# Performance work log

Measured on AMD Instinct MI355X. Metric: run time of the kernel, lower is better.

Reference implementation:

```python
import jax, jax.numpy as jnp
import numpy as np

NX, NY = 8192, 8192
FX, FY = 1024, 1024
EMB, EMB_OUT = 512, 512


def setup_inputs() -> dict:
    key = jax.random.key(0)
    ks = jax.random.split(key, 8)
    s = lambda f: 1.0 / np.sqrt(f)
    return {
        "x": jax.random.normal(ks[0], (NX, FX), jnp.float32),
        "y": jax.random.normal(ks[1], (NY, FY), jnp.float32),
        "Wx": jax.random.uniform(ks[2], (FX, EMB), jnp.float32, -s(FX), s(FX)),
        "bx": jax.random.uniform(ks[3], (EMB,), jnp.float32, -s(FX), s(FX)),
        "Wy": jax.random.uniform(ks[4], (FY, EMB), jnp.float32, -s(FY), s(FY)),
        "by": jax.random.uniform(ks[5], (EMB,), jnp.float32, -s(FY), s(FY)),
        "Wg": jax.random.uniform(ks[6], (EMB, EMB_OUT), jnp.float32, -s(EMB), s(EMB)),
        "bg": jax.random.uniform(ks[7], (EMB_OUT,), jnp.float32, -s(EMB), s(EMB)),
    }


def reference(x, y, Wx, bx, Wy, by, Wg, bg):
    # Linear projections: [Nx, emb], [Ny, emb]
    xp = x @ Wx + bx
    yp = y @ Wy + by
    # Pairwise affinity (Dice-coefficient style normalization)
    A_ = xp @ yp.T                              # [Nx, Ny]
    Dcol = jnp.sum(xp * xp, axis=1)[:, None]    # ||x_i||^2, diag of xp@xp.T
    Drow = jnp.sum(yp * yp, axis=1)[None, :]    # ||y_j||^2, diag of yp@yp.T
    A = 2.0 * A_ / (Dcol + Drow)                # [Nx, Ny]
    # Weighted aggregation over x nodes, then ReLU MLP
    gwf = A.T @ xp                              # [Ny, emb]
    return jax.nn.relu(gwf @ Wg + bg)           # [Ny, emb_out]
```

## Files before the change

kernel.cpp:

```cpp
#include <hip/hip_runtime.h>
#include <hip/hip_bf16.h>


typedef __attribute__((ext_vector_type(8))) short bf16x8;
typedef __attribute__((ext_vector_type(4))) short bf16x4;
typedef __attribute__((ext_vector_type(4))) float f32x4;

__device__ __forceinline__ short f2b(float f) {
    unsigned int u = __builtin_bit_cast(unsigned int, f);
    unsigned int r = (u + 0x7fffu + ((u >> 16) & 1u)) >> 16;
    return (short)r;
}
__device__ __forceinline__ float b2f(short s) {
    unsigned int u = ((unsigned int)(unsigned short)s) << 16;
    return __builtin_bit_cast(float, u);
}

__device__ __forceinline__ void cp16(const void* g, void* l) {
    __builtin_amdgcn_global_load_lds(
        (const __attribute__((address_space(1))) void*)g,
        (__attribute__((address_space(3))) void*)l, 16, 0, 0);
}

constexpr int EPI_XP = 0;
constexpr int EPI_BF = 1;
constexpr int EPI_AT = 2;

template<int EPI, int TM, int TN, int WVN>
__device__ __forceinline__ void gemm_core(
    const short* __restrict__ A, int lda,
    const short* __restrict__ Bt, int ldb,
    int N, int K, int bm, int bn, int kbase,
    const float* __restrict__ bias,
    short* __restrict__ outb,
    float* __restrict__ Dacc,
    const float* __restrict__ Drow, const float* __restrict__ Dcol)
{
    constexpr int WN  = WVN;
    constexpr int WM  = 4 / WN;
    constexpr int FRN = TN / WN / 16;
    constexpr int FRM = TM / WM / 16;
    __shared__ __align__(16) short As[TM * 32];
    __shared__ __align__(16) short Bs[TN * 32];

    const int tid  = threadIdx.x;
    const int wave = tid >> 6;
    const int lane = tid & 63;
    const int quad = lane >> 4;
    const int l15  = lane & 15;
    const int wn   = (wave % WN) * (FRN * 16);
    const int wm   = (wave / WN) * (FRM * 16);

    f32x4 acc[FRM][FRN];
#pragma unroll
    for (int i = 0; i < FRM; i++)
#pragma unroll
        for (int j = 0; j < FRN; j++) acc[i][j] = f32x4{0.f, 0.f, 0.f, 0.f};

    for (int k0 = kbase; k0 < kbase + K; k0 += 32) {
#pragma unroll
        for (int s = 0; s < TM / 64; s++) {
            const int seg = tid + 256 * s;
            const int row = seg >> 2, c8 = seg & 3;
            const int gg  = c8 ^ (row & 3);
            cp16(&A[(size_t)(bm + row) * lda + k0 + gg * 8], &As[seg * 8]);
        }
#pragma unroll
        for (int s = 0; s < TN / 64; s++) {
            const int seg = tid + 256 * s;
            const int row = seg >> 2, c8 = seg & 3;
            const int gg  = c8 ^ (row & 3);
            cp16(&Bt[(size_t)(bn + row) * ldb + k0 + gg * 8], &Bs[seg * 8]);
        }
        __syncthreads();

        bf16x8 a[FRM], b[FRN];
#pragma unroll
        for (int i = 0; i < FRM; i++) {
            const int row = wm + i * 16 + l15;
            a[i] = *(const bf16x8*)&As[row * 32 + ((quad ^ (row & 3)) << 3)];
        }
#pragma unroll
        for (int j = 0; j < FRN; j++) {
            const int row = wn + j * 16 + l15;
            b[j] = *(const bf16x8*)&Bs[row * 32 + ((quad ^ (row & 3)) << 3)];
        }
#pragma unroll
        for (int i = 0; i < FRM; i++)
#pragma unroll
            for (int j = 0; j < FRN; j++)
                acc[i][j] = __builtin_amdgcn_mfma_f32_16x16x32_bf16(a[i], b[j], acc[i][j], 0, 0, 0);
        __syncthreads();
    }

#pragma unroll
    for (int im = 0; im < FRM; ++im) {
#pragma unroll
        for (int r = 0; r < 4; ++r) {
            const int gm = bm + wm + im * 16 + quad * 4 + r;
            if (EPI == EPI_XP) {
                float s = 0.f;
#pragma unroll
                for (int jn = 0; jn < FRN; ++jn) {
                    const int gn = bn + wn + jn * 16 + l15;
                    const float v = acc[im][jn][r] + bias[gn];
                    outb[(size_t)gm * N + gn] = f2b(v);
                    s += v * v;
                }
#pragma unroll
                for (int m = 1; m < 16; m <<= 1) s += __shfl_xor(s, m, 64);
                if (l15 == 0) atomicAdd(&Dacc[gm], s);
            } else if (EPI == EPI_BF) {
#pragma unroll
                for (int jn = 0; jn < FRN; ++jn) {
                    const int gn = bn + wn + jn * 16 + l15;
                    outb[(size_t)gm * N + gn] = f2b(acc[im][jn][r]);
                }
            } else {
                const float dy = Drow[gm];
#pragma unroll
                for (int jn = 0; jn < FRN; ++jn) {
                    const int gn = bn + wn + jn * 16 + l15;
                    const float v = 2.f * acc[im][jn][r] * __builtin_amdgcn_rcpf(Dcol[gn] + dy);
                    outb[(size_t)gm * N + gn] = f2b(v);
                }
            }
        }
    }
}

__global__ __launch_bounds__(256)
void k_proj(const short* __restrict__ A, const short* __restrict__ Bt,
            const float* __restrict__ bias, short* __restrict__ outb,
            float* __restrict__ Dacc)
{
    gemm_core<EPI_XP, 64, 128, 2>(A, 1024, Bt, 1024, 512, 1024,
                                  blockIdx.y * 64, blockIdx.x * 128, 0,
                                  bias, outb, Dacc, nullptr, nullptr);
}

__global__ __launch_bounds__(256)
void k_zT(const short* __restrict__ WgT, const short* __restrict__ xpb,
          short* __restrict__ zT)
{
    gemm_core<EPI_BF, 64, 128, 2>(WgT, 512, xpb, 512, 8192, 512,
                                  blockIdx.y * 64, blockIdx.x * 128, 0,
                                  nullptr, zT, nullptr, nullptr, nullptr);
}

__global__ __launch_bounds__(256, 2)
void k_aff(const short* __restrict__ ypb, const short* __restrict__ xpb,
           short* __restrict__ At, const float* __restrict__ Dy,
           const float* __restrict__ Dx)
{
    const int flat = blockIdx.x;
    const int xcd = flat & 7;
    const int q   = flat >> 3;
    const int st  = q >> 5;
    const int w   = q & 31;
    const int s   = xcd * 8 + st;
    const int bx  = (s & 7) * 4 + (w & 3);
    const int by  = (s >> 3) * 8 + (w >> 2);
    gemm_core<EPI_AT, 128, 256, 2>(ypb, 512, xpb, 512, 8192, 512,
                                   by * 128, bx * 256, 0,
                                   nullptr, At, nullptr, Dy, Dx);
}

__global__ __launch_bounds__(256)
void k_agg(const short* __restrict__ At, const short* __restrict__ zT,
           short* __restrict__ p0, short* __restrict__ p1)
{
    const int flat = blockIdx.x;
    const int xcd = flat & 7;
    const int q   = flat >> 3;
    const int g   = xcd * 16 + (q >> 2);
    const int bm  = (g >> 1) * 128;
    const int z   = g & 1;
    const int bn  = (q & 3) * 128;
    short* outb = z ? p1 : p0;
    gemm_core<EPI_BF, 128, 128, 2>(At, 8192, zT, 8192, 512, 4096,
                                   bm, bn, z * 4096,
                                   nullptr, outb, nullptr, nullptr, nullptr);
}

__global__ __launch_bounds__(256)
void k_fin(const short* __restrict__ p0, const short* __restrict__ p1,
           const float* __restrict__ bg, float* __restrict__ out)
{
    const int idx = (blockIdx.x * 256 + threadIdx.x) * 8;
    const int col = idx & 511;
    const bf16x8 a = *(const bf16x8*)&p0[idx];
    const bf16x8 b = *(const bf16x8*)&p1[idx];
    const f32x4 g0 = *(const f32x4*)&bg[col];
    const f32x4 g1 = *(const f32x4*)&bg[col + 4];
    f32x4 o0, o1;
#pragma unroll
    for (int e = 0; e < 4; ++e) {
        o0[e] = fmaxf(b2f(a[e]) + b2f(b[e]) + g0[e], 0.f);
        o1[e] = fmaxf(b2f(a[e + 4]) + b2f(b[e + 4]) + g1[e], 0.f);
    }
    *(f32x4*)&out[idx]     = o0;
    *(f32x4*)&out[idx + 4] = o1;
}

__global__ __launch_bounds__(256)
void k_cvt(const float* __restrict__ in, short* __restrict__ out)
{
    const int i = (blockIdx.x * 256 + threadIdx.x) * 4;
    const float4 v = *(const float4*)&in[i];
    bf16x4 b;
    b[0] = f2b(v.x); b[1] = f2b(v.y); b[2] = f2b(v.z); b[3] = f2b(v.w);
    *(bf16x4*)&out[i] = b;
}

__global__ __launch_bounds__(256)
void transpose_f32_bf16(const float* __restrict__ in, short* __restrict__ out, int R, int C)
{
    __shared__ short t[32][33];
    const int tx = threadIdx.x, ty = threadIdx.y;
    const int bx = blockIdx.x * 32, by = blockIdx.y * 32;
#pragma unroll
    for (int i = 0; i < 32; i += 8)
        t[ty + i][tx] = f2b(in[(size_t)(by + ty + i) * C + bx + tx]);
    __syncthreads();
#pragma unroll
    for (int i = 0; i < 32; i += 8)
        out[(size_t)(bx + ty + i) * R + by + tx] = t[tx][ty + i];
}

extern "C" void kernel_launch(void* const* d_in, const int* in_sizes, int n_in,
                              void* d_out, int out_size, void* d_ws, size_t ws_size,
                              hipStream_t stream)
{
    const float* x  = (const float*)d_in[0];
    const float* y  = (const float*)d_in[1];
    const float* Wx = (const float*)d_in[2];
    const float* bx = (const float*)d_in[3];
    const float* Wy = (const float*)d_in[4];
    const float* by = (const float*)d_in[5];
    const float* Wg = (const float*)d_in[6];
    const float* bg = (const float*)d_in[7];
    float* out = (float*)d_out;

    char* p = (char*)d_ws;
    short* At   = (short*)p;
    short* xb   = (short*)p;
    short* yb   = (short*)(p + (size_t)8192 * 1024 * 2);
    p += (size_t)8192 * 8192 * 2;
    short* xpb  = (short*)p; p += (size_t)8192 * 512 * 2;
    short* ypb  = (short*)p; p += (size_t)8192 * 512 * 2;
    short* zT   = (short*)p; p += (size_t)512 * 8192 * 2;
    short* WxT  = (short*)p; p += (size_t)512 * 1024 * 2;
    short* WyT  = (short*)p; p += (size_t)512 * 1024 * 2;
    short* WgT  = (short*)p; p += (size_t)512 * 512 * 2;
    float* Dx   = (float*)p; p += (size_t)8192 * 4;
    float* Dy   = (float*)p; p += (size_t)8192 * 4;
    short* p0 = xpb;
    short* p1 = ypb;

    hipMemsetAsync(Dx, 0, 2 * 8192 * sizeof(float), stream);

    dim3 tb(32, 8);
    transpose_f32_bf16<<<dim3(512 / 32, 1024 / 32), tb, 0, stream>>>(Wx, WxT, 1024, 512);
    transpose_f32_bf16<<<dim3(512 / 32, 1024 / 32), tb, 0, stream>>>(Wy, WyT, 1024, 512);
    transpose_f32_bf16<<<dim3(512 / 32, 512 / 32),  tb, 0, stream>>>(Wg, WgT, 512, 512);

    k_cvt<<<8192, 256, 0, stream>>>(x, xb);
    k_cvt<<<8192, 256, 0, stream>>>(y, yb);

    k_proj<<<dim3(4, 128), 256, 0, stream>>>(xb, WxT, bx, xpb, Dx);
    k_proj<<<dim3(4, 128), 256, 0, stream>>>(yb, WyT, by, ypb, Dy);

    k_zT<<<dim3(64, 8), 256, 0, stream>>>(WgT, xpb, zT);

    k_aff<<<2048, 256, 0, stream>>>(ypb, xpb, At, Dy, Dx);

    k_agg<<<512, 256, 0, stream>>>(At, zT, p0, p1);

    k_fin<<<2048, 256, 0, stream>>>(p0, p1, bg, out);
}
```

Baseline: 356.0 us.

## Add deep multi-buffered LDS pipeline GEMM for affinity and aggregation kernels

```diff
diff --git a/kernel.cpp b/kernel.cpp
--- a/kernel.cpp
+++ b/kernel.cpp
@@ -20,6 +20,15 @@
     __builtin_amdgcn_global_load_lds(
         (const __attribute__((address_space(1))) void*)g,
         (__attribute__((address_space(3))) void*)l, 16, 0, 0);
+}
+
+template<int N>
+__device__ __forceinline__ void waitvm() {
+    if constexpr (N == 0)      asm volatile("s_waitcnt vmcnt(0)" ::: "memory");
+    else if constexpr (N == 4) asm volatile("s_waitcnt vmcnt(4)" ::: "memory");
+    else if constexpr (N == 6) asm volatile("s_waitcnt vmcnt(6)" ::: "memory");
+    else if constexpr (N == 8) asm volatile("s_waitcnt vmcnt(8)" ::: "memory");
+    else static_assert(N == 0, "unsupported vmcnt literal");
 }
 
 constexpr int EPI_XP = 0;
@@ -110,19 +119,132 @@
 #pragma unroll
                 for (int m = 1; m < 16; m <<= 1) s += __shfl_xor(s, m, 64);
                 if (l15 == 0) atomicAdd(&Dacc[gm], s);
-            } else if (EPI == EPI_BF) {
+            } else {
 #pragma unroll
                 for (int jn = 0; jn < FRN; ++jn) {
                     const int gn = bn + wn + jn * 16 + l15;
                     outb[(size_t)gm * N + gn] = f2b(acc[im][jn][r]);
                 }
-            } else {
+            }
+        }
+    }
+}
+
+template<int EPI, int TM, int TN, int RING>
+__device__ __forceinline__ void gemm_deep(
+    const short* __restrict__ A, int lda,
+    const short* __restrict__ Bt, int ldb,
+    int N, int K, int bm, int bn, int kbase,
+    short* __restrict__ outb,
+    const float* __restrict__ Drow, const float* __restrict__ Dcol)
+{
+    constexpr int FRM = TM / 32;
+    constexpr int FRN = TN / 32;
+    constexpr int CPA = TM * 4 / 256;
+    constexpr int CPB = TN * 4 / 256;
+    constexpr int CPT = CPA + CPB;
+    __shared__ __align__(16) short As[RING][TM * 32];
+    __shared__ __align__(16) short Bs[RING][TN * 32];
+
+    const int tid  = threadIdx.x;
+    const int wave = tid >> 6;
+    const int lane = tid & 63;
+    const int quad = lane >> 4;
+    const int l15  = lane & 15;
+    const int wm   = (wave >> 1) * (FRM * 16);
+    const int wn   = (wave & 1) * (FRN * 16);
+    const int nk   = K / 32;
+
+    f32x4 acc[FRM][FRN];
+#pragma unroll
+    for (int i = 0; i < FRM; i++)
+#pragma unroll
+        for (int j = 0; j < FRN; j++) acc[i][j] = f32x4{0.f, 0.f, 0.f, 0.f};
+
+    auto stage = [&](int slot, int t) {
+        const int k0 = kbase + t * 32;
+#pragma unroll
+        for (int s = 0; s < CPA; s++) {
+            const int seg = tid + 256 * s;
+            const int row = seg >> 2, c8 = seg & 3;
+            const int gg  = c8 ^ (row & 3);
+            cp16(&A[(size_t)(bm + row) * lda + k0 + gg * 8], &As[slot][seg * 8]);
+        }
+#pragma unroll
+        for (int s = 0; s < CPB; s++) {
+            const int seg = tid + 256 * s;
+            const int row = seg >> 2, c8 = seg & 3;
+            const int gg  = c8 ^ (row & 3);
+            cp16(&Bt[(size_t)(bn + row) * ldb + k0 + gg * 8], &Bs[slot][seg * 8]);
+        }
+    };
+
+#pragma unroll
+    for (int p = 0; p < RING - 1; ++p) stage(p, p);
+
+    int cur = 0, prv = RING - 1;
+    for (int t = 0; t < nk; ++t) {
+        if constexpr (RING == 3) {
+            if (t + 1 < nk) waitvm<CPT>(); else waitvm<0>();
+        } else {
+            if (t + 2 < nk)      waitvm<2 * CPT>();
+            else if (t + 1 < nk) waitvm<CPT>();
+            else                 waitvm<0>();
+        }
+        __builtin_amdgcn_s_barrier();
+        if (t + RING - 1 < nk) stage(prv, t + RING - 1);
+
+        bf16x8 a[FRM], b[FRN];
+#pragma unroll
+        for (int i = 0; i < FRM; i++) {
+            const int row = wm + i * 16 + l15;
+            a[i] = *(const bf16x8*)&As[cur][row * 32 + ((quad ^ (row & 3)) << 3)];
+        }
+#pragma unroll
+        for (int j = 0; j < FRN; j++) {
+            const int row = wn + j * 16 + l15;
+            b[j] = *(const bf16x8*)&Bs[cur][row * 32 + ((quad ^ (row & 3)) << 3)];
+        }
+        __builtin_amdgcn_s_setprio(1);
+#pragma unroll
+        for (int i = 0; i < FRM; i++)
+#pragma unroll
+            for (int j = 0; j < FRN; j++)
+                acc[i][j] = __builtin_amdgcn_mfma_f32_16x16x32_bf16(a[i], b[j], acc[i][j], 0, 0, 0);
+        __builtin_amdgcn_s_setprio(0);
+        asm volatile("s_waitcnt lgkmcnt(0)" ::: "memory");
+        prv = cur;
+        cur = (cur + 1 == RING) ? 0 : cur + 1;
+    }
+
+    if (EPI == EPI_AT) {
+        float dcol[FRN];
+#pragma unroll
+        for (int jn = 0; jn < FRN; ++jn) dcol[jn] = Dcol[bn + wn + jn * 16 + l15];
+#pragma unroll
+        for (int im = 0; im < FRM; ++im) {
+#pragma unroll
+            for (int r = 0; r < 4; ++r) {
+                const int gm = bm + wm + im * 16 + quad * 4 + r;
                 const float dy = Drow[gm];
 #pragma unroll
                 for (int jn = 0; jn < FRN; ++jn) {
                     const int gn = bn + wn + jn * 16 + l15;
-                    const float v = 2.f * acc[im][jn][r] * __builtin_amdgcn_rcpf(Dcol[gn] + dy);
+                    const float v = 2.f * acc[im][jn][r] * __builtin_amdgcn_rcpf(dcol[jn] + dy);
                     outb[(size_t)gm * N + gn] = f2b(v);
+                }
+            }
+        }
+    } else {
+#pragma unroll
+        for (int im = 0; im < FRM; ++im) {
+#pragma unroll
+            for (int r = 0; r < 4; ++r) {
+                const int gm = bm + wm + im * 16 + quad * 4 + r;
+#pragma unroll
+                for (int jn = 0; jn < FRN; ++jn) {
+                    const int gn = bn + wn + jn * 16 + l15;
+                    outb[(size_t)gm * N + gn] = f2b(acc[im][jn][r]);
                 }
             }
         }
@@ -156,17 +278,13 @@
     const int flat = blockIdx.x;
     const int xcd = flat & 7;
     const int q   = flat >> 3;
-    const int st  = q >> 5;
-    const int w   = q & 31;
-    const int s   = xcd * 8 + st;
-    const int bx  = (s & 7) * 4 + (w & 3);
-    const int by  = (s >> 3) * 8 + (w >> 2);
-    gemm_core<EPI_AT, 128, 256, 2>(ypb, 512, xpb, 512, 8192, 512,
-                                   by * 128, bx * 256, 0,
-                                   nullptr, At, nullptr, Dy, Dx);
-}
-
-__global__ __launch_bounds__(256)
+    const int by  = xcd * 4 + (q & 3);
+    const int bx  = q >> 2;
+    gemm_deep<EPI_AT, 256, 128, 3>(ypb, 512, xpb, 512, 8192, 512,
+                                   by * 256, bx * 128, 0, At, Dy, Dx);
+}
+
+__global__ __launch_bounds__(256, 2)
 void k_agg(const short* __restrict__ At, const short* __restrict__ zT,
            short* __restrict__ p0, short* __restrict__ p1)
 {
@@ -178,9 +296,8 @@
     const int z   = g & 1;
     const int bn  = (q & 3) * 128;
     short* outb = z ? p1 : p0;
-    gemm_core<EPI_BF, 128, 128, 2>(At, 8192, zT, 8192, 512, 4096,
-                                   bm, bn, z * 4096,
-                                   nullptr, outb, nullptr, nullptr, nullptr);
+    gemm_deep<EPI_BF, 128, 128, 4>(At, 8192, zT, 8192, 512, 4096,
+                                   bm, bn, z * 4096, outb, nullptr, nullptr);
 }
 
 __global__ __launch_bounds__(256)
```

Measured after the change: 356.1 us. About the same (+0.0%).

## Add multi-stage LDS ring pipelining to GEMMs and merge small launches

Applied to the files above, without the earlier changes.

```diff
diff --git a/kernel.cpp b/kernel.cpp
--- a/kernel.cpp
+++ b/kernel.cpp
@@ -22,12 +22,26 @@
         (__attribute__((address_space(3))) void*)l, 16, 0, 0);
 }
 
+template<int N>
+__device__ __forceinline__ void waitvm() {
+    if constexpr (N == 0)      asm volatile("s_waitcnt vmcnt(0)" ::: "memory");
+    else if constexpr (N == 3) asm volatile("s_waitcnt vmcnt(3)" ::: "memory");
+    else if constexpr (N == 4) asm volatile("s_waitcnt vmcnt(4)" ::: "memory");
+    else if constexpr (N == 6) asm volatile("s_waitcnt vmcnt(6)" ::: "memory");
+    else if constexpr (N == 8) asm volatile("s_waitcnt vmcnt(8)" ::: "memory");
+    else static_assert(N == 0, "unsupported vmcnt literal");
+}
+
+__device__ __forceinline__ int gslot(int c, int row) {
+    return c ^ (row & 3) ^ ((row >> 2) & 3);
+}
+
 constexpr int EPI_XP = 0;
 constexpr int EPI_BF = 1;
 constexpr int EPI_AT = 2;
 
-template<int EPI, int TM, int TN, int WVN>
-__device__ __forceinline__ void gemm_core(
+template<int EPI, int TM, int TN, int RING>
+__device__ __forceinline__ void gemm_deep(
     const short* __restrict__ A, int lda,
     const short* __restrict__ Bt, int ldb,
     int N, int K, int bm, int bn, int kbase,
@@ -36,20 +50,22 @@
     float* __restrict__ Dacc,
     const float* __restrict__ Drow, const float* __restrict__ Dcol)
 {
-    constexpr int WN  = WVN;
-    constexpr int WM  = 4 / WN;
-    constexpr int FRN = TN / WN / 16;
-    constexpr int FRM = TM / WM / 16;
-    __shared__ __align__(16) short As[TM * 32];
-    __shared__ __align__(16) short Bs[TN * 32];
+    constexpr int FRM = TM / 32;
+    constexpr int FRN = TN / 32;
+    constexpr int CPA = TM * 4 / 256;
+    constexpr int CPB = TN * 4 / 256;
+    constexpr int CPT = CPA + CPB;
+    __shared__ __align__(16) short As[RING][TM * 32];
+    __shared__ __align__(16) short Bs[RING][TN * 32];
 
     const int tid  = threadIdx.x;
     const int wave = tid >> 6;
     const int lane = tid & 63;
     const int quad = lane >> 4;
     const int l15  = lane & 15;
-    const int wn   = (wave % WN) * (FRN * 16);
-    const int wm   = (wave / WN) * (FRM * 16);
+    const int wm   = (wave >> 1) * (FRM * 16);
+    const int wn   = (wave & 1) * (FRN * 16);
+    const int nk   = K / 32;
 
     f32x4 acc[FRM][FRN];
 #pragma unroll
@@ -57,40 +73,69 @@
 #pragma unroll
         for (int j = 0; j < FRN; j++) acc[i][j] = f32x4{0.f, 0.f, 0.f, 0.f};
 
-    for (int k0 = kbase; k0 < kbase + K; k0 += 32) {
-#pragma unroll
-        for (int s = 0; s < TM / 64; s++) {
+    auto stage = [&](int slot, int t) {
+        const int k0 = kbase + t * 32;
+#pragma unroll
+        for (int s = 0; s < CPA; s++) {
             const int seg = tid + 256 * s;
             const int row = seg >> 2, c8 = seg & 3;
-            const int gg  = c8 ^ (row & 3);
-            cp16(&A[(size_t)(bm + row) * lda + k0 + gg * 8], &As[seg * 8]);
-        }
-#pragma unroll
-        for (int s = 0; s < TN / 64; s++) {
+            const int gg  = gslot(c8, row);
+            cp16(&A[(size_t)(bm + row) * lda + k0 + gg * 8], &As[slot][seg * 8]);
+        }
+#pragma unroll
+        for (int s = 0; s < CPB; s++) {
             const int seg = tid + 256 * s;
             const int row = seg >> 2, c8 = seg & 3;
-            const int gg  = c8 ^ (row & 3);
-            cp16(&Bt[(size_t)(bn + row) * ldb + k0 + gg * 8], &Bs[seg * 8]);
-        }
-        __syncthreads();
-
-        bf16x8 a[FRM], b[FRN];
+            const int gg  = gslot(c8, row);
+            cp16(&Bt[(size_t)(bn + row) * ldb + k0 + gg * 8], &Bs[slot][seg * 8]);
+        }
+    };
+
+    bf16x8 a[FRM], b[FRN];
+    auto ldfrag = [&](int slot) {
 #pragma unroll
         for (int i = 0; i < FRM; i++) {
             const int row = wm + i * 16 + l15;
-            a[i] = *(const bf16x8*)&As[row * 32 + ((quad ^ (row & 3)) << 3)];
+            a[i] = *(const bf16x8*)&As[slot][row * 32 + (gslot(quad, row) << 3)];
         }
 #pragma unroll
         for (int j = 0; j < FRN; j++) {
             const int row = wn + j * 16 + l15;
-            b[j] = *(const bf16x8*)&Bs[row * 32 + ((quad ^ (row & 3)) << 3)];
-        }
+            b[j] = *(const bf16x8*)&Bs[slot][row * 32 + (gslot(quad, row) << 3)];
+        }
+    };
+
+#pragma unroll
+    for (int p = 0; p < RING - 1; ++p) stage(p, p);
+    waitvm<(RING - 2) * CPT>();
+    ldfrag(0);
+
+    int cur = 0, prv = RING - 1;
+    for (int t = 0; t < nk; ++t) {
+        __builtin_amdgcn_s_barrier();
+        if (t + RING - 1 < nk) stage(prv, t + RING - 1);
+
+        __builtin_amdgcn_s_setprio(1);
 #pragma unroll
         for (int i = 0; i < FRM; i++)
 #pragma unroll
             for (int j = 0; j < FRN; j++)
                 acc[i][j] = __builtin_amdgcn_mfma_f32_16x16x32_bf16(a[i], b[j], acc[i][j], 0, 0, 0);
-        __syncthreads();
+        __builtin_amdgcn_s_setprio(0);
+        __builtin_amdgcn_sched_barrier(0);
+
+        if (t + 1 < nk) {
+            if constexpr (RING == 3) {
+                if (t + 2 < nk) waitvm<CPT>(); else waitvm<0>();
+            } else {
+                if (t + 3 < nk)      waitvm<2 * CPT>();
+                else if (t + 2 < nk) waitvm<CPT>();
+                else                 waitvm<0>();
+            }
+            ldfrag((cur + 1 == RING) ? 0 : cur + 1);
+        }
+        prv = cur;
+        cur = (cur + 1 == RING) ? 0 : cur + 1;
     }
 
 #pragma unroll
@@ -110,13 +155,7 @@
 #pragma unroll
                 for (int m = 1; m < 16; m <<= 1) s += __shfl_xor(s, m, 64);
                 if (l15 == 0) atomicAdd(&Dacc[gm], s);
-            } else if (EPI == EPI_BF) {
-#pragma unroll
-                for (int jn = 0; jn < FRN; ++jn) {
-                    const int gn = bn + wn + jn * 16 + l15;
-                    outb[(size_t)gm * N + gn] = f2b(acc[im][jn][r]);
-                }
-            } else {
+            } else if (EPI == EPI_AT) {
                 const float dy = Drow[gm];
 #pragma unroll
                 for (int jn = 0; jn < FRN; ++jn) {
@@ -124,6 +163,12 @@
                     const float v = 2.f * acc[im][jn][r] * __builtin_amdgcn_rcpf(Dcol[gn] + dy);
                     outb[(size_t)gm * N + gn] = f2b(v);
                 }
+            } else {
+#pragma unroll
+                for (int jn = 0; jn < FRN; ++jn) {
+                    const int gn = bn + wn + jn * 16 + l15;
+                    outb[(size_t)gm * N + gn] = f2b(acc[im][jn][r]);
+                }
             }
         }
     }
@@ -134,7 +179,7 @@
             const float* __restrict__ bias, short* __restrict__ outb,
             float* __restrict__ Dacc)
 {
-    gemm_core<EPI_XP, 64, 128, 2>(A, 1024, Bt, 1024, 512, 1024,
+    gemm_deep<EPI_XP, 64, 128, 4>(A, 1024, Bt, 1024, 512, 1024,
                                   blockIdx.y * 64, blockIdx.x * 128, 0,
                                   bias, outb, Dacc, nullptr, nullptr);
 }
@@ -143,7 +188,7 @@
 void k_zT(const short* __restrict__ WgT, const short* __restrict__ xpb,
           short* __restrict__ zT)
 {
-    gemm_core<EPI_BF, 64, 128, 2>(WgT, 512, xpb, 512, 8192, 512,
+    gemm_deep<EPI_BF, 64, 128, 4>(WgT, 512, xpb, 512, 8192, 512,
                                   blockIdx.y * 64, blockIdx.x * 128, 0,
                                   nullptr, zT, nullptr, nullptr, nullptr);
 }
@@ -156,17 +201,14 @@
     const int flat = blockIdx.x;
     const int xcd = flat & 7;
     const int q   = flat >> 3;
-    const int st  = q >> 5;
-    const int w   = q & 31;
-    const int s   = xcd * 8 + st;
-    const int bx  = (s & 7) * 4 + (w & 3);
-    const int by  = (s >> 3) * 8 + (w >> 2);
-    gemm_core<EPI_AT, 128, 256, 2>(ypb, 512, xpb, 512, 8192, 512,
-                                   by * 128, bx * 256, 0,
+    const int by  = xcd * 4 + (q & 3);
+    const int bx  = q >> 2;
+    gemm_deep<EPI_AT, 256, 128, 3>(ypb, 512, xpb, 512, 8192, 512,
+                                   by * 256, bx * 128, 0,
                                    nullptr, At, nullptr, Dy, Dx);
 }
 
-__global__ __launch_bounds__(256)
+__global__ __launch_bounds__(256, 2)
 void k_agg(const short* __restrict__ At, const short* __restrict__ zT,
            short* __restrict__ p0, short* __restrict__ p1)
 {
@@ -178,7 +220,7 @@
     const int z   = g & 1;
     const int bn  = (q & 3) * 128;
     short* outb = z ? p1 : p0;
-    gemm_core<EPI_BF, 128, 128, 2>(At, 8192, zT, 8192, 512, 4096,
+    gemm_deep<EPI_BF, 128, 128, 4>(At, 8192, zT, 8192, 512, 4096,
                                    bm, bn, z * 4096,
                                    nullptr, outb, nullptr, nullptr, nullptr);
 }
@@ -204,8 +246,11 @@
 }
 
 __global__ __launch_bounds__(256)
-void k_cvt(const float* __restrict__ in, short* __restrict__ out)
-{
+void k_cvt(const float* __restrict__ x, const float* __restrict__ y,
+           short* __restrict__ xb, short* __restrict__ yb)
+{
+    const float* in  = blockIdx.y ? y  : x;
+    short*       out = blockIdx.y ? yb : xb;
     const int i = (blockIdx.x * 256 + threadIdx.x) * 4;
     const float4 v = *(const float4*)&in[i];
     bf16x4 b;
@@ -213,8 +258,8 @@
     *(bf16x4*)&out[i] = b;
 }
 
-__global__ __launch_bounds__(256)
-void transpose_f32_bf16(const float* __restrict__ in, short* __restrict__ out, int R, int C)
+__device__ __forceinline__ void transpose_body(
+    const float* __restrict__ in, short* __restrict__ out, int R, int C)
 {
     __shared__ short t[32][33];
     const int tx = threadIdx.x, ty = threadIdx.y;
@@ -226,6 +271,19 @@
 #pragma unroll
     for (int i = 0; i < 32; i += 8)
         out[(size_t)(bx + ty + i) * R + by + tx] = t[tx][ty + i];
+}
+
+__global__ __launch_bounds__(256)
+void t_wxy(const float* __restrict__ Wx, const float* __restrict__ Wy,
+           short* __restrict__ WxT, short* __restrict__ WyT)
+{
+    transpose_body(blockIdx.z ? Wy : Wx, blockIdx.z ? WyT : WxT, 1024, 512);
+}
+
+__global__ __launch_bounds__(256)
+void t_wg(const float* __restrict__ Wg, short* __restrict__ WgT)
+{
+    transpose_body(Wg, WgT, 512, 512);
 }
 
 extern "C" void kernel_launch(void* const* d_in, const int* in_sizes, int n_in,
@@ -261,12 +319,10 @@
     hipMemsetAsync(Dx, 0, 2 * 8192 * sizeof(float), stream);
 
     dim3 tb(32, 8);
-    transpose_f32_bf16<<<dim3(512 / 32, 1024 / 32), tb, 0, stream>>>(Wx, WxT, 1024, 512);
-    transpose_f32_bf16<<<dim3(512 / 32, 1024 / 32), tb, 0, stream>>>(Wy, WyT, 1024, 512);
-    transpose_f32_bf16<<<dim3(512 / 32, 512 / 32),  tb, 0, stream>>>(Wg, WgT, 512, 512);
-
-    k_cvt<<<8192, 256, 0, stream>>>(x, xb);
-    k_cvt<<<8192, 256, 0, stream>>>(y, yb);
+    t_wxy<<<dim3(16, 32, 2), tb, 0, stream>>>(Wx, Wy, WxT, WyT);
+    t_wg<<<dim3(16, 16), tb, 0, stream>>>(Wg, WgT);
+
+    k_cvt<<<dim3(8192, 2), 256, 0, stream>>>(x, y, xb, yb);
 
     k_proj<<<dim3(4, 128), 256, 0, stream>>>(xb, WxT, bx, xpb, Dx);
     k_proj<<<dim3(4, 128), 256, 0, stream>>>(yb, WyT, by, ypb, Dy);
```

After: 333.3 us. 1.07x faster.
